# Optimization experiments

Measured on AMD Instinct MI355X. Metric: run time of the kernel, lower is better.

The kernel has to match this reference:

```python
import jax, jax.numpy as jnp
import numpy as np

DIM = 2048
N_HEADS = 16
N_KV_HEADS = 4
HEAD_DIM = DIM // N_HEADS  # 128
N_REP = N_HEADS // N_KV_HEADS
LENS = [1024, 2048, 512, 512]
T = sum(LENS)  # 4096 packed tokens
THETA = 10000.0
NEG_INF = -1e30


def setup_inputs() -> dict:
    key = jax.random.key(0)
    ks = jax.random.split(key, 5)
    sd = 1.0 / np.sqrt(DIM)
    x = jax.random.normal(ks[0], (T, DIM), dtype=jnp.float32)
    wq = jax.random.normal(ks[1], (DIM, N_HEADS * HEAD_DIM), dtype=jnp.float32) * sd
    wk = jax.random.normal(ks[2], (DIM, N_KV_HEADS * HEAD_DIM), dtype=jnp.float32) * sd
    wv = jax.random.normal(ks[3], (DIM, N_KV_HEADS * HEAD_DIM), dtype=jnp.float32) * sd
    wo = jax.random.normal(ks[4], (N_HEADS * HEAD_DIM, DIM), dtype=jnp.float32) * sd
    # varlen packing metadata: per-token segment id and in-sequence position
    seq_ids = jnp.asarray(np.repeat(np.arange(len(LENS)), LENS), dtype=jnp.int32)
    pos = jnp.asarray(np.concatenate([np.arange(l) for l in LENS]), dtype=jnp.float32)
    # rotary frequencies (precompute_freqs_cis), gathered per packed token
    inv_freq = 1.0 / (THETA ** (np.arange(0, HEAD_DIM, 2, dtype=np.float32) / HEAD_DIM))  # [HEAD_DIM//2]
    angles = pos[:, None] * jnp.asarray(inv_freq)[None, :]  # [T, HEAD_DIM//2]
    freqs_cos = jnp.cos(angles)
    freqs_sin = jnp.sin(angles)
    return {"x": x, "wq": wq, "wk": wk, "wv": wv, "wo": wo,
            "freqs_cos": freqs_cos, "freqs_sin": freqs_sin, "seq_ids": seq_ids}


def _apply_rope(t, cos, sin):
    # t: [T, H, D]; rotate interleaved (even, odd) pairs, matching torch view_as_complex
    tr = t.reshape(t.shape[0], t.shape[1], HEAD_DIM // 2, 2)
    x0, x1 = tr[..., 0], tr[..., 1]
    c = cos[:, None, :]
    s = sin[:, None, :]
    o0 = x0 * c - x1 * s
    o1 = x0 * s + x1 * c
    return jnp.stack([o0, o1], axis=-1).reshape(t.shape)


def reference(x, wq, wk, wv, wo, freqs_cos, freqs_sin, seq_ids):
    Tn = x.shape[0]
    xq = (x @ wq).reshape(Tn, N_HEADS, HEAD_DIM)
    xk = (x @ wk).reshape(Tn, N_KV_HEADS, HEAD_DIM)
    xv = (x @ wv).reshape(Tn, N_KV_HEADS, HEAD_DIM)
    xq = _apply_rope(xq, freqs_cos, freqs_sin)
    xk = _apply_rope(xk, freqs_cos, freqs_sin)
    # GQA: repeat kv heads
    xk = jnp.repeat(xk, N_REP, axis=1)  # [T, N_HEADS, D]
    xv = jnp.repeat(xv, N_REP, axis=1)
    scale = 1.0 / jnp.sqrt(jnp.float32(HEAD_DIM))
    scores = jnp.einsum('thd,shd->hts', xq, xk) * scale  # [H, T, T]
    idx = jnp.arange(Tn)
    # varlen causal mask: same sequence AND key index <= query index
    allowed = (seq_ids[:, None] == seq_ids[None, :]) & (idx[None, :] <= idx[:, None])
    scores = jnp.where(allowed[None, :, :], scores, NEG_INF)
    attn = jax.nn.softmax(scores, axis=-1)
    out = jnp.einsum('hts,shd->thd', attn, xv).reshape(Tn, N_HEADS * HEAD_DIM)
    return out @ wo
```

## Files before the change

kernel.cpp:

```cpp
#include <hip/hip_runtime.h>
#include <hip/hip_bf16.h>


typedef __attribute__((ext_vector_type(4))) float f32x4;
typedef __attribute__((ext_vector_type(8))) short short8;
typedef __attribute__((ext_vector_type(4))) short short4v;

#define DEV __device__ __forceinline__

DEV short f2bf(float f) {
  __hip_bfloat16 h = __float2bfloat16(f);
  union { __hip_bfloat16 h; short s; } u; u.h = h; return u.s;
}
DEV float bf2f(short s) {
  union { short s; __hip_bfloat16 h; } u; u.s = s; return __bfloat162float(u.h);
}

DEV void gload_lds16(const void* g, void* l) {
  __builtin_amdgcn_global_load_lds(
      (const __attribute__((address_space(1))) void*)g,
      (__attribute__((address_space(3))) void*)l, 16, 0, 0);
}

__global__ void cast_x(const float* __restrict__ in, short* __restrict__ out, int n4) {
  int i = blockIdx.x * 256 + threadIdx.x;
  if (i >= n4) return;
  f32x4 v = ((const f32x4*)in)[i];
  short4v o;
  o[0] = f2bf(v[0]); o[1] = f2bf(v[1]); o[2] = f2bf(v[2]); o[3] = f2bf(v[3]);
  ((short4v*)out)[i] = o;
}

__global__ void transpose_cast_f32(const float* __restrict__ in, short* __restrict__ out,
                                   int R, int C) {
  __shared__ float tile[32][33];
  int bc = blockIdx.x * 32, br = blockIdx.y * 32;
  int tx = threadIdx.x, ty = threadIdx.y;
#pragma unroll
  for (int i = 0; i < 32; i += 8)
    tile[ty + i][tx] = in[(size_t)(br + ty + i) * C + bc + tx];
  __syncthreads();
#pragma unroll
  for (int i = 0; i < 32; i += 8)
    out[(size_t)(bc + ty + i) * R + br + tx] = f2bf(tile[tx][ty + i]);
}

__global__ void transpose_bf16(const short* __restrict__ in, short* __restrict__ out,
                               int R, int C, int ldi, int ldo) {
  __shared__ short tile[32][33];
  int bc = blockIdx.x * 32, br = blockIdx.y * 32;
  int tx = threadIdx.x, ty = threadIdx.y;
#pragma unroll
  for (int i = 0; i < 32; i += 8)
    tile[ty + i][tx] = in[(size_t)(br + ty + i) * ldi + bc + tx];
  __syncthreads();
#pragma unroll
  for (int i = 0; i < 32; i += 8)
    out[(size_t)(bc + ty + i) * ldo + br + tx] = tile[tx][ty + i];
}

__global__ void rope_kernel(short* __restrict__ qkv,
                            const float* __restrict__ fc, const float* __restrict__ fs) {
  int t = blockIdx.x;
  int g = threadIdx.x;
  int gi, col;
  if (g < 256) { int h = g >> 4; gi = g & 15; col = h * 128 + gi * 8; }
  else { int kh = (g - 256) >> 4; gi = (g - 256) & 15; col = 2048 + kh * 128 + gi * 8; }
  size_t base = (size_t)t * 3072 + col;
  short8 v = *(short8*)(qkv + base);
  f32x4 c = *(const f32x4*)(fc + (size_t)t * 64 + gi * 4);
  f32x4 s = *(const f32x4*)(fs + (size_t)t * 64 + gi * 4);
#pragma unroll
  for (int e = 0; e < 4; ++e) {
    float x0 = bf2f(v[2 * e]), x1 = bf2f(v[2 * e + 1]);
    float o0 = x0 * c[e] - x1 * s[e];
    float o1 = x0 * s[e] + x1 * c[e];
    v[2 * e] = f2bf(o0); v[2 * e + 1] = f2bf(o1);
  }
  *(short8*)(qkv + base) = v;
}

template <typename OutT>
__global__ __launch_bounds__(256, 2) void gemm_bt(const short* __restrict__ A,
                                                  const short* __restrict__ BT,
                                                  OutT* __restrict__ C,
                                                  int M, int N, int K,
                                                  int lda, int ldb, int ldc) {
  __shared__ short As[128 * 32];
  __shared__ short Bs[128 * 32];
  const int tid = threadIdx.x;
  const int wave = tid >> 6, lane = tid & 63;
  const int wr = wave >> 1, wc = wave & 1;
  const int bm = blockIdx.y, bn = blockIdx.x;
  const int l15 = lane & 15, l4 = lane >> 4;
  f32x4 acc[4][4] = {};
  for (int kt = 0; kt < K; kt += 32) {
    __syncthreads();
#pragma unroll
    for (int i = 0; i < 2; ++i) {
      int j = wave * 2 + i;
      int row = j * 16 + (lane >> 2);
      int lg = (lane & 3) ^ ((row >> 1) & 3);
      gload_lds16(A + (size_t)(bm * 128 + row) * lda + kt + lg * 8, As + j * 512);
      gload_lds16(BT + (size_t)(bn * 128 + row) * ldb + kt + lg * 8, Bs + j * 512);
    }
    __syncthreads();
    short8 a[4], b[4];
#pragma unroll
    for (int m = 0; m < 4; ++m) {
      int row = wr * 64 + m * 16 + l15;
      int ph = l4 ^ ((row >> 1) & 3);
      a[m] = *(const short8*)(As + row * 32 + ph * 8);
    }
#pragma unroll
    for (int n = 0; n < 4; ++n) {
      int row = wc * 64 + n * 16 + l15;
      int ph = l4 ^ ((row >> 1) & 3);
      b[n] = *(const short8*)(Bs + row * 32 + ph * 8);
    }
#pragma unroll
    for (int m = 0; m < 4; ++m)
#pragma unroll
      for (int n = 0; n < 4; ++n)
        acc[m][n] = __builtin_amdgcn_mfma_f32_16x16x32_bf16(a[m], b[n], acc[m][n], 0, 0, 0);
  }
#pragma unroll
  for (int m = 0; m < 4; ++m) {
    int row0 = bm * 128 + wr * 64 + m * 16 + l4 * 4;
#pragma unroll
    for (int n = 0; n < 4; ++n) {
      int col = bn * 128 + wc * 64 + n * 16 + l15;
#pragma unroll
      for (int r = 0; r < 4; ++r) {
        float v = acc[m][n][r];
        if constexpr (sizeof(OutT) == 4) C[(size_t)(row0 + r) * ldc + col] = v;
        else                             C[(size_t)(row0 + r) * ldc + col] = f2bf(v);
      }
    }
  }
}


__constant__ int QPERM[64] = {
    47, 46, 45, 44, 43, 42, 41, 40, 39, 38, 37, 36, 35, 34, 33, 32,
    31, 15, 30, 14, 29, 13, 28, 12, 27, 11, 26, 10, 25,  9, 24,  8,
    23,  7, 55, 63, 22,  6, 54, 62, 21,  5, 53, 61, 20,  4, 52, 60,
    19,  3, 51, 59, 18,  2, 50, 58, 17,  1, 49, 57, 16,  0, 48, 56};

__global__ __launch_bounds__(256, 2) void attn_kernel(const short* __restrict__ qkv,
                                                      const short* __restrict__ vt,
                                                      short* __restrict__ out) {
  __shared__ short Ks[2][64 * 128];
  __shared__ short Vs[2][128 * 64];
  __shared__ short Ps[4][16 * 64];
  const int tid = threadIdx.x;
  const int wave = tid >> 6, lane = tid & 63;
  const int l15 = lane & 15, l4 = lane >> 4;
  const int h = blockIdx.x;
  const int qi = QPERM[blockIdx.y];
  const int q0 = qi * 64;
  const int kvh = h >> 2;

  const int trow = q0 + wave * 16 + l15;
  short8 qf[4];
#pragma unroll
  for (int kk = 0; kk < 4; ++kk)
    qf[kk] = *(const short8*)(qkv + (size_t)trow * 3072 + h * 128 + kk * 32 + l4 * 8);

  f32x4 of[8] = {};
  float mrun[4], lrun[4];
#pragma unroll
  for (int r = 0; r < 4; ++r) { mrun[r] = -1e30f; lrun[r] = 0.f; }

  const int kstart = (q0 >= 3584) ? 3584 : (q0 >= 3072) ? 3072 : (q0 >= 1024) ? 1024 : 0;
  const int nt = ((q0 + 64) - kstart) >> 6;
  short* Pw = Ps[wave];

  auto stage = [&](int buf, int kt) {
    short* Kb = &Ks[buf][0];
    short* Vb = &Vs[buf][0];
#pragma unroll
    for (int j = 0; j < 4; ++j) {
      int krow = j * 16 + wave * 4 + (lane >> 4);
      int ksl = (lane & 15) ^ (krow & 7);
      gload_lds16(qkv + (size_t)(kt + krow) * 3072 + 2048 + kvh * 128 + ksl * 8,
                  Kb + (j * 16 + wave * 4) * 128);
      int vrow = j * 32 + wave * 8 + (lane >> 3);
      int vsl = (lane & 7) ^ (vrow & 7);
      gload_lds16(vt + (size_t)(kvh * 128 + vrow) * 4096 + kt + vsl * 8,
                  Vb + (j * 32 + wave * 8) * 64);
    }
  };

  stage(0, kstart);
  __syncthreads();

  constexpr float SCL2 = 0.08838834764831845f * 1.4426950408889634f;

  for (int ti = 0; ti < nt; ++ti) {
    const int kt = kstart + ti * 64;
    const int cur = ti & 1;
    if (ti + 1 < nt) stage(cur ^ 1, kt + 64);

    const short* Kb = &Ks[cur][0];
    const short* Vb = &Vs[cur][0];

    f32x4 sfr[4] = {};
    __builtin_amdgcn_s_setprio(1);
#pragma unroll
    for (int st = 0; st < 4; ++st) {
      int srow = st * 16 + l15;
#pragma unroll
      for (int kk = 0; kk < 4; ++kk) {
        int ph = (kk * 4 + l4) ^ (srow & 7);
        short8 kfrag = *(const short8*)(Kb + srow * 128 + ph * 8);
        sfr[st] = __builtin_amdgcn_mfma_f32_16x16x32_bf16(qf[kk], kfrag, sfr[st], 0, 0, 0);
      }
    }
    __builtin_amdgcn_s_setprio(0);

    float p[4][4];
#pragma unroll
    for (int r = 0; r < 4; ++r) {
      int tg = q0 + wave * 16 + l4 * 4 + r;
      float v[4];
#pragma unroll
      for (int st = 0; st < 4; ++st) {
        v[st] = sfr[st][r] * SCL2;
        if (kt + st * 16 + l15 > tg) v[st] = -1e30f;
      }
      float mx = fmaxf(fmaxf(v[0], v[1]), fmaxf(v[2], v[3]));
#pragma unroll
      for (int off = 1; off < 16; off <<= 1) mx = fmaxf(mx, __shfl_xor(mx, off));
      float mn = fmaxf(mrun[r], mx);
      float scl = __builtin_amdgcn_exp2f(mrun[r] - mn);
      float sum = 0.f;
#pragma unroll
      for (int st = 0; st < 4; ++st) {
        p[st][r] = __builtin_amdgcn_exp2f(v[st] - mn);
        sum += p[st][r];
      }
#pragma unroll
      for (int off = 1; off < 16; off <<= 1) sum += __shfl_xor(sum, off);
      lrun[r] = lrun[r] * scl + sum;
      mrun[r] = mn;
#pragma unroll
      for (int nd = 0; nd < 8; ++nd) of[nd][r] *= scl;
    }

#pragma unroll
    for (int st = 0; st < 4; ++st)
#pragma unroll
      for (int r = 0; r < 4; ++r) {
        int row = l4 * 4 + r;
        int col = st * 16 + l15;
        int ph = (col >> 3) ^ (row & 7);
        Pw[row * 64 + ph * 8 + (col & 7)] = f2bf(p[st][r]);
      }

    __builtin_amdgcn_s_setprio(1);
#pragma unroll
    for (int kc = 0; kc < 2; ++kc) {
      int pph = (kc * 4 + l4) ^ (l15 & 7);
      short8 pa = *(const short8*)(Pw + l15 * 64 + pph * 8);
#pragma unroll
      for (int nd = 0; nd < 8; ++nd) {
        int vrow = nd * 16 + l15;
        int vph = (kc * 4 + l4) ^ (vrow & 7);
        short8 vf = *(const short8*)(Vb + vrow * 64 + vph * 8);
        of[nd] = __builtin_amdgcn_mfma_f32_16x16x32_bf16(pa, vf, of[nd], 0, 0, 0);
      }
    }
    __builtin_amdgcn_s_setprio(0);

    __syncthreads();
  }

#pragma unroll
  for (int r = 0; r < 4; ++r) {
    float inv = 1.0f / lrun[r];
    int tg = q0 + wave * 16 + l4 * 4 + r;
#pragma unroll
    for (int nd = 0; nd < 8; ++nd)
      out[(size_t)tg * 2048 + h * 128 + nd * 16 + l15] = f2bf(of[nd][r] * inv);
  }
}

extern "C" void kernel_launch(void* const* d_in, const int* in_sizes, int n_in,
                              void* d_out, int out_size, void* d_ws, size_t ws_size,
                              hipStream_t stream) {
  (void)in_sizes; (void)n_in; (void)out_size; (void)ws_size;
  const float* x  = (const float*)d_in[0];
  const float* wq = (const float*)d_in[1];
  const float* wk = (const float*)d_in[2];
  const float* wv = (const float*)d_in[3];
  const float* wo = (const float*)d_in[4];
  const float* fc = (const float*)d_in[5];
  const float* fs = (const float*)d_in[6];

  char* p = (char*)d_ws;
  short* xb  = (short*)p; p += (size_t)4096 * 2048 * 2;
  short* wT  = (short*)p; p += (size_t)3072 * 2048 * 2;
  short* woT = (short*)p; p += (size_t)2048 * 2048 * 2;
  short* qkv = (short*)p; p += (size_t)4096 * 3072 * 2;
  short* vt  = (short*)p; p += (size_t)512 * 4096 * 2;
  short* ao  = (short*)p; p += (size_t)4096 * 2048 * 2;
  float* outp = (float*)d_out;

  dim3 tb(32, 8);
  cast_x<<<8192, 256, 0, stream>>>(x, xb, 2097152);
  transpose_cast_f32<<<dim3(64, 64), tb, 0, stream>>>(wq, wT,               2048, 2048);
  transpose_cast_f32<<<dim3(16, 64), tb, 0, stream>>>(wk, wT + 2048 * 2048, 2048, 512);
  transpose_cast_f32<<<dim3(16, 64), tb, 0, stream>>>(wv, wT + 2560 * 2048, 2048, 512);
  transpose_cast_f32<<<dim3(64, 64), tb, 0, stream>>>(wo, woT,              2048, 2048);
  gemm_bt<short><<<dim3(24, 32), 256, 0, stream>>>(xb, wT, qkv, 4096, 3072, 2048,
                                                   2048, 2048, 3072);
  rope_kernel<<<4096, 320, 0, stream>>>(qkv, fc, fs);
  transpose_bf16<<<dim3(16, 128), tb, 0, stream>>>(qkv + 2560, vt, 4096, 512, 3072, 4096);
  attn_kernel<<<dim3(16, 64), 256, 0, stream>>>(qkv, vt, ao);
  gemm_bt<float><<<dim3(16, 32), 256, 0, stream>>>(ao, woT, outp, 4096, 2048, 2048,
                                                   2048, 2048, 2048);
}
```

Before: 320.6 us.

## Double-buffer GEMM LDS, register-staged attention loads, lazy softmax rescale, more occupancy

The GEMM now double-buffers its LDS tiles, so the next K-slice is fetched while MFMAs run on the current one, and it raises wave priority around the MFMA block. The attention kernel drops its double LDS buffers in favour of prefetching K/V into registers, writing them to single LDS buffers after compute. This halves attention LDS and raises launch bounds to 4 blocks per CU. Softmax now rescales the running max and accumulators only when a new max exceeds the old by more than 8 (log2 units), skipping most rescale work. The trade-offs are an extra barrier per attention tile, extra register pressure from the prefetch, and lazy rescaling that lets un-normalised exponentials grow up to 2^8.

```diff
diff --git a/kernel.cpp b/kernel.cpp
--- a/kernel.cpp
+++ b/kernel.cpp
@@ -86,44 +86,57 @@
                                                   OutT* __restrict__ C,
                                                   int M, int N, int K,
                                                   int lda, int ldb, int ldc) {
-  __shared__ short As[128 * 32];
-  __shared__ short Bs[128 * 32];
+  __shared__ short As[2][128 * 32];
+  __shared__ short Bs[2][128 * 32];
   const int tid = threadIdx.x;
   const int wave = tid >> 6, lane = tid & 63;
   const int wr = wave >> 1, wc = wave & 1;
   const int bm = blockIdx.y, bn = blockIdx.x;
   const int l15 = lane & 15, l4 = lane >> 4;
   f32x4 acc[4][4] = {};
-  for (int kt = 0; kt < K; kt += 32) {
-    __syncthreads();
+
+  auto stage = [&](int buf, int kt) {
 #pragma unroll
     for (int i = 0; i < 2; ++i) {
       int j = wave * 2 + i;
       int row = j * 16 + (lane >> 2);
       int lg = (lane & 3) ^ ((row >> 1) & 3);
-      gload_lds16(A + (size_t)(bm * 128 + row) * lda + kt + lg * 8, As + j * 512);
-      gload_lds16(BT + (size_t)(bn * 128 + row) * ldb + kt + lg * 8, Bs + j * 512);
-    }
-    __syncthreads();
+      gload_lds16(A + (size_t)(bm * 128 + row) * lda + kt + lg * 8, &As[buf][j * 512]);
+      gload_lds16(BT + (size_t)(bn * 128 + row) * ldb + kt + lg * 8, &Bs[buf][j * 512]);
+    }
+  };
+
+  stage(0, 0);
+  __syncthreads();
+
+  const int nk = K >> 5;
+  for (int t = 0; t < nk; ++t) {
+    const int cur = t & 1;
+    if (t + 1 < nk) stage(cur ^ 1, (t + 1) * 32);
+
     short8 a[4], b[4];
 #pragma unroll
     for (int m = 0; m < 4; ++m) {
       int row = wr * 64 + m * 16 + l15;
       int ph = l4 ^ ((row >> 1) & 3);
-      a[m] = *(const short8*)(As + row * 32 + ph * 8);
+      a[m] = *(const short8*)(&As[cur][row * 32 + ph * 8]);
     }
 #pragma unroll
     for (int n = 0; n < 4; ++n) {
       int row = wc * 64 + n * 16 + l15;
       int ph = l4 ^ ((row >> 1) & 3);
-      b[n] = *(const short8*)(Bs + row * 32 + ph * 8);
-    }
+      b[n] = *(const short8*)(&Bs[cur][row * 32 + ph * 8]);
+    }
+    __builtin_amdgcn_s_setprio(1);
 #pragma unroll
     for (int m = 0; m < 4; ++m)
 #pragma unroll
       for (int n = 0; n < 4; ++n)
         acc[m][n] = __builtin_amdgcn_mfma_f32_16x16x32_bf16(a[m], b[n], acc[m][n], 0, 0, 0);
-  }
+    __builtin_amdgcn_s_setprio(0);
+    __syncthreads();
+  }
+
 #pragma unroll
   for (int m = 0; m < 4; ++m) {
     int row0 = bm * 128 + wr * 64 + m * 16 + l4 * 4;
@@ -147,11 +160,11 @@
     23,  7, 55, 63, 22,  6, 54, 62, 21,  5, 53, 61, 20,  4, 52, 60,
     19,  3, 51, 59, 18,  2, 50, 58, 17,  1, 49, 57, 16,  0, 48, 56};
 
-__global__ __launch_bounds__(256, 2) void attn_kernel(const short* __restrict__ qkv,
+__global__ __launch_bounds__(256, 4) void attn_kernel(const short* __restrict__ qkv,
                                                       const short* __restrict__ vt,
                                                       short* __restrict__ out) {
-  __shared__ short Ks[2][64 * 128];
-  __shared__ short Vs[2][128 * 64];
+  __shared__ short Ks[64 * 128];
+  __shared__ short Vs[128 * 64];
   __shared__ short Ps[4][16 * 64];
   const int tid = threadIdx.x;
   const int wave = tid >> 6, lane = tid & 63;
@@ -176,34 +189,38 @@
   const int nt = ((q0 + 64) - kstart) >> 6;
   short* Pw = Ps[wave];
 
-  auto stage = [&](int buf, int kt) {
-    short* Kb = &Ks[buf][0];
-    short* Vb = &Vs[buf][0];
+  const int krow0 = wave * 4 + (lane >> 4);
+  const int ksl   = (lane & 15) ^ (krow0 & 7);
+  const int vrow0 = wave * 8 + (lane >> 3);
+  const int vsl   = (lane & 7) ^ (vrow0 & 7);
+
+  short8 kreg[4], vreg[4];
+  auto load_regs = [&](int kt) {
 #pragma unroll
     for (int j = 0; j < 4; ++j) {
-      int krow = j * 16 + wave * 4 + (lane >> 4);
-      int ksl = (lane & 15) ^ (krow & 7);
-      gload_lds16(qkv + (size_t)(kt + krow) * 3072 + 2048 + kvh * 128 + ksl * 8,
-                  Kb + (j * 16 + wave * 4) * 128);
-      int vrow = j * 32 + wave * 8 + (lane >> 3);
-      int vsl = (lane & 7) ^ (vrow & 7);
-      gload_lds16(vt + (size_t)(kvh * 128 + vrow) * 4096 + kt + vsl * 8,
-                  Vb + (j * 32 + wave * 8) * 64);
+      kreg[j] = *(const short8*)(qkv + (size_t)(kt + j * 16 + krow0) * 3072 + 2048 +
+                                 kvh * 128 + ksl * 8);
+      vreg[j] = *(const short8*)(vt + (size_t)(kvh * 128 + j * 32 + vrow0) * 4096 + kt +
+                                 vsl * 8);
     }
   };
-
-  stage(0, kstart);
+  auto write_lds = [&]() {
+#pragma unroll
+    for (int j = 0; j < 4; ++j) {
+      *(short8*)(Ks + (j * 16 + krow0) * 128 + (lane & 15) * 8) = kreg[j];
+      *(short8*)(Vs + (j * 32 + vrow0) * 64 + (lane & 7) * 8) = vreg[j];
+    }
+  };
+
+  load_regs(kstart);
+  write_lds();
   __syncthreads();
 
   constexpr float SCL2 = 0.08838834764831845f * 1.4426950408889634f;
 
   for (int ti = 0; ti < nt; ++ti) {
     const int kt = kstart + ti * 64;
-    const int cur = ti & 1;
-    if (ti + 1 < nt) stage(cur ^ 1, kt + 64);
-
-    const short* Kb = &Ks[cur][0];
-    const short* Vb = &Vs[cur][0];
+    if (ti + 1 < nt) load_regs(kt + 64);
 
     f32x4 sfr[4] = {};
     __builtin_amdgcn_s_setprio(1);
@@ -213,39 +230,52 @@
 #pragma unroll
       for (int kk = 0; kk < 4; ++kk) {
         int ph = (kk * 4 + l4) ^ (srow & 7);
-        short8 kfrag = *(const short8*)(Kb + srow * 128 + ph * 8);
+        short8 kfrag = *(const short8*)(Ks + srow * 128 + ph * 8);
         sfr[st] = __builtin_amdgcn_mfma_f32_16x16x32_bf16(qf[kk], kfrag, sfr[st], 0, 0, 0);
       }
     }
     __builtin_amdgcn_s_setprio(0);
 
-    float p[4][4];
+    float p[4][4], mx[4];
 #pragma unroll
     for (int r = 0; r < 4; ++r) {
       int tg = q0 + wave * 16 + l4 * 4 + r;
-      float v[4];
+      float m = -1e30f;
 #pragma unroll
       for (int st = 0; st < 4; ++st) {
-        v[st] = sfr[st][r] * SCL2;
-        if (kt + st * 16 + l15 > tg) v[st] = -1e30f;
-      }
-      float mx = fmaxf(fmaxf(v[0], v[1]), fmaxf(v[2], v[3]));
-#pragma unroll
-      for (int off = 1; off < 16; off <<= 1) mx = fmaxf(mx, __shfl_xor(mx, off));
-      float mn = fmaxf(mrun[r], mx);
-      float scl = __builtin_amdgcn_exp2f(mrun[r] - mn);
+        float v = sfr[st][r] * SCL2;
+        if (kt + st * 16 + l15 > tg) v = -1e30f;
+        p[st][r] = v;
+        m = fmaxf(m, v);
+      }
+#pragma unroll
+      for (int off = 1; off < 16; off <<= 1) m = fmaxf(m, __shfl_xor(m, off));
+      mx[r] = m;
+    }
+    bool need = (mx[0] > mrun[0] + 8.f) || (mx[1] > mrun[1] + 8.f) ||
+                (mx[2] > mrun[2] + 8.f) || (mx[3] > mrun[3] + 8.f);
+    if (__any(need)) {
+#pragma unroll
+      for (int r = 0; r < 4; ++r) {
+        float mn = fmaxf(mrun[r], mx[r]);
+        float scl = __builtin_amdgcn_exp2f(mrun[r] - mn);
+        lrun[r] *= scl;
+        mrun[r] = mn;
+#pragma unroll
+        for (int nd = 0; nd < 8; ++nd) of[nd][r] *= scl;
+      }
+    }
+#pragma unroll
+    for (int r = 0; r < 4; ++r) {
       float sum = 0.f;
 #pragma unroll
       for (int st = 0; st < 4; ++st) {
-        p[st][r] = __builtin_amdgcn_exp2f(v[st] - mn);
+        p[st][r] = __builtin_amdgcn_exp2f(p[st][r] - mrun[r]);
         sum += p[st][r];
       }
 #pragma unroll
       for (int off = 1; off < 16; off <<= 1) sum += __shfl_xor(sum, off);
-      lrun[r] = lrun[r] * scl + sum;
-      mrun[r] = mn;
-#pragma unroll
-      for (int nd = 0; nd < 8; ++nd) of[nd][r] *= scl;
+      lrun[r] += sum;
     }
 
 #pragma unroll
@@ -267,12 +297,14 @@
       for (int nd = 0; nd < 8; ++nd) {
         int vrow = nd * 16 + l15;
         int vph = (kc * 4 + l4) ^ (vrow & 7);
-        short8 vf = *(const short8*)(Vb + vrow * 64 + vph * 8);
+        short8 vf = *(const short8*)(Vs + vrow * 64 + vph * 8);
         of[nd] = __builtin_amdgcn_mfma_f32_16x16x32_bf16(pa, vf, of[nd], 0, 0, 0);
       }
     }
     __builtin_amdgcn_s_setprio(0);
 
+    __syncthreads();
+    if (ti + 1 < nt) write_lds();
     __syncthreads();
   }
 
```

New measurement: 494.0 us. 1.54x slower.
